# Performance work log

Measured on AMD Instinct MI355X. Metric: run time of the kernel, lower is better.

Reference implementation:

```python
import jax, jax.numpy as jnp
import numpy as np

KERNELSIZE = 9


def generate_pe(pos_num, d_num):
    pos = jnp.arange(pos_num, dtype=jnp.float32)[:, None]
    d_i = jnp.arange(0, d_num + 1, 2, dtype=jnp.float32)[None, :]
    ang = pos / jnp.power(jnp.float32(10000.0), d_i / d_num)  # [pos, ceil((d+1)/2)]
    pe = jnp.zeros((pos_num, d_num), dtype=jnp.float32)
    n_even = pe[:, 0::2].shape[1]
    n_odd = pe[:, 1::2].shape[1]
    pe = pe.at[:, 0::2].set(jnp.sin(ang)[:, :n_even])
    pe = pe.at[:, 1::2].set(jnp.cos(ang)[:, :n_odd])
    return pe


def nearest_idx(in_size, out_size):
    # torch F.interpolate(mode='nearest'): src = floor(dst * in/out)
    return jnp.floor(jnp.arange(out_size) * (in_size / out_size)).astype(jnp.int32)


def setup_inputs() -> dict:
    N, K, C_in, C_out, ks = 30000, 16, 256, 128, KERNELSIZE
    key = jax.random.key(0)
    k0, k1, k2, k3, k4, k5, k6, k7 = jax.random.split(key, 8)
    return {
        "ndata": jax.random.normal(k0, (N, C_in), jnp.float32),
        "neighbors": jax.random.randint(k1, (N, K), 0, N),
        "W_lin": jax.random.normal(k2, (C_out, C_in), jnp.float32) * 0.05,
        "b_lin": jax.random.normal(k3, (C_out,), jnp.float32) * 0.05,
        "weight": jax.random.normal(k4, (C_out, ks), jnp.float32),
        "bias": jax.random.normal(k5, (C_out,), jnp.float32),
        "W_res": jax.random.normal(k6, (C_out, C_in), jnp.float32) * 0.05,
        "b_res": jax.random.normal(k7, (C_out,), jnp.float32) * 0.05,
    }


def reference(ndata, neighbors, W_lin, b_lin, weight, bias, W_res, b_res):
    N = ndata.shape[0]
    C_out, ks = weight.shape
    feat = ndata @ W_lin.T + b_lin                              # [N, D]
    # mailbox = in-neighbor features + self-loop (dgl.add_self_loop)
    mailbox = jnp.concatenate([feat[neighbors], feat[:, None, :]], axis=1)  # [N, S, D]
    S = mailbox.shape[1]
    x = jnp.sort(mailbox, axis=1)                                # sort along neighbor dim
    idx = nearest_idx(ks, S)
    pe = generate_pe(ks, C_out)                                  # [ks, D]
    x = x + pe[idx][None, :, :]                                  # interpolated PE
    w_local = weight[:, idx].T                                   # [S, D] interpolated weight
    Xf = jnp.fft.fft(x, axis=1)
    Wf = jnp.fft.fft(w_local, axis=0)
    y = jnp.fft.ifft(Xf * jnp.conj(Wf)[None, :, :], axis=1).real  # circular correlation
    h = y.sum(axis=1) + bias                                     # [N, D]
    return h + ndata @ W_res.T + b_res
```

## Files before the change

kernel.cpp:

```cpp
#include <hip/hip_runtime.h>
#include <math.h>

#define N_NODES 30000
#define K_NBR   16
#define C_IN    256
#define C_OUT   128
#define KS      9
#define S_MB    17

typedef __attribute__((ext_vector_type(4))) float f32x4;
typedef __attribute__((ext_vector_type(8))) short bf16x8;

static __device__ __forceinline__ ushort f2bf(float f) {
    uint u = __builtin_bit_cast(uint, f);
    u += 0x7fffu + ((u >> 16) & 1u);
    return (ushort)(u >> 16);
}

__global__ __launch_bounds__(256)
void pcg_prep(const float* __restrict__ W_lin,
              const float* __restrict__ W_res,
              const float* __restrict__ weight,
              const float* __restrict__ b_lin,
              const float* __restrict__ bias,
              const float* __restrict__ b_res,
              ushort* __restrict__ Bf,
              float* __restrict__ Ws,
              float* __restrict__ Cd) {
    if (blockIdx.x == 32) {
        int d = threadIdx.x;
        if (d >= C_OUT) return;
        float freq = powf(10000.0f, -(float)(d & ~1) / (float)C_OUT);
        float ws = 0.f, p = 0.f;
        for (int s = 0; s < S_MB; ++s) {
            int idx = (int)floorf((float)s * (9.0f / 17.0f));
            ws += weight[d * KS + idx];
            float ang = (float)idx * freq;
            p += (d & 1) ? cosf(ang) : sinf(ang);
        }
        Ws[d] = ws;
        Cd[d] = ws * ((float)(K_NBR + 1) * b_lin[d] + p) + bias[d] + b_res[d];
        return;
    }
    const int tt     = blockIdx.x * 256 + threadIdx.x;
    const int col_lo = tt & 15;
    const int ksub   = (tt >> 4) & 3;
    const int colhi  = (tt >> 6) & 15;
    const int kc     = tt >> 10;
    const int col    = colhi * 16 + col_lo;
    const int k0     = kc * 32 + ksub * 8;
    const float* Wr = (col < C_OUT)
        ? &W_lin[(size_t)col * C_IN + k0]
        : &W_res[(size_t)(col - C_OUT) * C_IN + k0];
    const float4 w0 = *reinterpret_cast<const float4*>(Wr);
    const float4 w1 = *reinterpret_cast<const float4*>(Wr + 4);
    ushort b[8] = { f2bf(w0.x), f2bf(w0.y), f2bf(w0.z), f2bf(w0.w),
                    f2bf(w1.x), f2bf(w1.y), f2bf(w1.z), f2bf(w1.w) };
    *reinterpret_cast<uint4*>(&Bf[(size_t)tt * 8]) =
        *reinterpret_cast<const uint4*>(b);
}

__global__ __launch_bounds__(256)
void pcg_mfma(const float* __restrict__ ndata,
              const ushort* __restrict__ Bf,
              ushort* __restrict__ F) {
    __shared__ short sA[16384];

    const int t  = threadIdx.x;
    const int n0 = blockIdx.x * 64;

#pragma unroll
    for (int i = 0; i < 16; ++i) {
        const int v    = i * 256 + t;
        const int row  = v >> 6;
        const int k0   = (v & 63) * 4;
        float4 a = make_float4(0.f, 0.f, 0.f, 0.f);
        if (n0 + row < N_NODES)
            a = *reinterpret_cast<const float4*>(
                    &ndata[(size_t)(n0 + row) * C_IN + k0]);
        const int kc   = k0 >> 5;
        const int rg   = row >> 4;
        const int l    = (row & 15) | (((k0 >> 3) & 3) << 4);
        const int half = (k0 >> 2) & 1;
        uint2 w;
        w.x = (uint)f2bf(a.x) | ((uint)f2bf(a.y) << 16);
        w.y = (uint)f2bf(a.z) | ((uint)f2bf(a.w) << 16);
        *reinterpret_cast<uint2*>(&sA[(kc * 4 + rg) * 512 + l * 8 + half * 4]) = w;
    }
    __syncthreads();

    const int wave = t >> 6;
    const int l    = t & 63;

    f32x4 acc[4][4] = {};

#pragma unroll
    for (int kc = 0; kc < 8; ++kc) {
        bf16x8 a[4];
#pragma unroll
        for (int rg = 0; rg < 4; ++rg)
            a[rg] = *reinterpret_cast<const bf16x8*>(
                        &sA[(kc * 4 + rg) * 512 + l * 8]);
        bf16x8 b[4];
#pragma unroll
        for (int cg = 0; cg < 4; ++cg)
            b[cg] = *reinterpret_cast<const bf16x8*>(
                        &Bf[((size_t)(kc * 16 + wave * 4 + cg) * 64 + l) * 8]);
#pragma unroll
        for (int rg = 0; rg < 4; ++rg)
#pragma unroll
            for (int cg = 0; cg < 4; ++cg)
                acc[rg][cg] = __builtin_amdgcn_mfma_f32_16x16x32_bf16(
                                  a[rg], b[cg], acc[rg][cg], 0, 0, 0);
    }

    const int colw = wave * 64 + (l & 15);
    const int rl   = (l >> 4) * 4;
#pragma unroll
    for (int rg = 0; rg < 4; ++rg) {
#pragma unroll
        for (int cg = 0; cg < 4; ++cg) {
            const int col = colw + cg * 16;
#pragma unroll
            for (int j = 0; j < 4; ++j) {
                const int row = n0 + rg * 16 + rl + j;
                if (row < N_NODES)
                    F[(size_t)row * 256 + col] = f2bf(acc[rg][cg][j]);
            }
        }
    }
}

__global__ __launch_bounds__(256)
void pcg_gather(const int* __restrict__ neighbors,
                const ushort* __restrict__ F,
                const float* __restrict__ Ws,
                const float* __restrict__ Cd,
                float* __restrict__ out) {
    __shared__ int snb[64];
    const int t = threadIdx.x;
    if (t < 64) snb[t] = neighbors[(size_t)blockIdx.x * 64 + t];
    __syncthreads();

    const int g = t >> 6;
    const int l = t & 63;
    const int n = blockIdx.x * 4 + g;

    const ushort* Frow = F + (size_t)n * 256;
    uint u = *reinterpret_cast<const uint*>(&Frow[2 * l]);
    float a0 = __builtin_bit_cast(float, u << 16);
    float a1 = __builtin_bit_cast(float, u & 0xffff0000u);

#pragma unroll
    for (int k = 0; k < K_NBR; ++k) {
        const int m = snb[g * 16 + k];
        uint v = *reinterpret_cast<const uint*>(&F[(size_t)m * 256 + 2 * l]);
        a0 += __builtin_bit_cast(float, v << 16);
        a1 += __builtin_bit_cast(float, v & 0xffff0000u);
    }

    uint r = *reinterpret_cast<const uint*>(&Frow[128 + 2 * l]);
    float r0 = __builtin_bit_cast(float, r << 16);
    float r1 = __builtin_bit_cast(float, r & 0xffff0000u);

    float2 ws = *reinterpret_cast<const float2*>(&Ws[2 * l]);
    float2 cd = *reinterpret_cast<const float2*>(&Cd[2 * l]);

    float2 o;
    o.x = ws.x * a0 + r0 + cd.x;
    o.y = ws.y * a1 + r1 + cd.y;
    *reinterpret_cast<float2*>(&out[(size_t)n * C_OUT + 2 * l]) = o;
}

extern "C" void kernel_launch(void* const* d_in, const int* in_sizes, int n_in,
                              void* d_out, int out_size, void* d_ws, size_t ws_size,
                              hipStream_t stream) {
    const float* ndata     = (const float*)d_in[0];
    const int*   neighbors = (const int*)  d_in[1];
    const float* W_lin     = (const float*)d_in[2];
    const float* b_lin     = (const float*)d_in[3];
    const float* weight    = (const float*)d_in[4];
    const float* bias      = (const float*)d_in[5];
    const float* W_res     = (const float*)d_in[6];
    const float* b_res     = (const float*)d_in[7];
    float* out = (float*)d_out;

    ushort* F  = (ushort*)d_ws;
    ushort* Bf = F + (size_t)N_NODES * 256;
    float*  Ws = (float*)(Bf + 65536);
    float*  Cd = Ws + C_OUT;

    pcg_prep<<<33, 256, 0, stream>>>(W_lin, W_res, weight, b_lin, bias, b_res,
                                     Bf, Ws, Cd);
    pcg_mfma<<<(N_NODES + 63) / 64, 256, 0, stream>>>(ndata, Bf, F);
    pcg_gather<<<N_NODES / 4, 256, 0, stream>>>(neighbors, F, Ws, Cd, out);
}
```

Before: 43.84 us.

## Fold Ws scale, residual and constant into GEMM epilogue; gather pre-scaled rows

The GEMM epilogue now multiplies the linear output by the per-channel weight sum and writes two bf16 arrays: the scaled neighbour features and a per-node term that already includes the self contribution, the residual and the constants. Column groups are remapped so each wave holds matching linear and residual columns. The gather kernel then only sums pre-scaled rows and stores with nontemporal writes, dropping the residual and Ws/Cd loads. Nontemporal loads are also used for ndata. Output bytes stay the same, but the extra bf16 rounding after scaling changes numerical error slightly.

```diff
diff --git a/kernel.cpp b/kernel.cpp
--- a/kernel.cpp
+++ b/kernel.cpp
@@ -9,6 +9,7 @@
 #define S_MB    17
 
 typedef __attribute__((ext_vector_type(4))) float f32x4;
+typedef __attribute__((ext_vector_type(2))) float f32x2;
 typedef __attribute__((ext_vector_type(8))) short bf16x8;
 
 static __device__ __forceinline__ ushort f2bf(float f) {
@@ -52,8 +53,8 @@
     const float* Wr = (col < C_OUT)
         ? &W_lin[(size_t)col * C_IN + k0]
         : &W_res[(size_t)(col - C_OUT) * C_IN + k0];
-    const float4 w0 = *reinterpret_cast<const float4*>(Wr);
-    const float4 w1 = *reinterpret_cast<const float4*>(Wr + 4);
+    const f32x4 w0 = *reinterpret_cast<const f32x4*>(Wr);
+    const f32x4 w1 = *reinterpret_cast<const f32x4*>(Wr + 4);
     ushort b[8] = { f2bf(w0.x), f2bf(w0.y), f2bf(w0.z), f2bf(w0.w),
                     f2bf(w1.x), f2bf(w1.y), f2bf(w1.z), f2bf(w1.w) };
     *reinterpret_cast<uint4*>(&Bf[(size_t)tt * 8]) =
@@ -63,7 +64,10 @@
 __global__ __launch_bounds__(256)
 void pcg_mfma(const float* __restrict__ ndata,
               const ushort* __restrict__ Bf,
-              ushort* __restrict__ F) {
+              const float* __restrict__ Ws,
+              const float* __restrict__ Cd,
+              ushort* __restrict__ Gs,
+              ushort* __restrict__ Pc) {
     __shared__ short sA[16384];
 
     const int t  = threadIdx.x;
@@ -74,10 +78,10 @@
         const int v    = i * 256 + t;
         const int row  = v >> 6;
         const int k0   = (v & 63) * 4;
-        float4 a = make_float4(0.f, 0.f, 0.f, 0.f);
+        f32x4 a = {0.f, 0.f, 0.f, 0.f};
         if (n0 + row < N_NODES)
-            a = *reinterpret_cast<const float4*>(
-                    &ndata[(size_t)(n0 + row) * C_IN + k0]);
+            a = __builtin_nontemporal_load(reinterpret_cast<const f32x4*>(
+                    &ndata[(size_t)(n0 + row) * C_IN + k0]));
         const int kc   = k0 >> 5;
         const int rg   = row >> 4;
         const int l    = (row & 15) | (((k0 >> 3) & 3) << 4);
@@ -92,6 +96,11 @@
     const int wave = t >> 6;
     const int l    = t & 63;
 
+    const int ch0 = 2 * wave;
+    const int ch1 = 2 * wave + 1;
+    const int ch2 = 8 + 2 * wave;
+    const int ch3 = 9 + 2 * wave;
+
     f32x4 acc[4][4] = {};
 
 #pragma unroll
@@ -102,10 +111,10 @@
             a[rg] = *reinterpret_cast<const bf16x8*>(
                         &sA[(kc * 4 + rg) * 512 + l * 8]);
         bf16x8 b[4];
-#pragma unroll
-        for (int cg = 0; cg < 4; ++cg)
-            b[cg] = *reinterpret_cast<const bf16x8*>(
-                        &Bf[((size_t)(kc * 16 + wave * 4 + cg) * 64 + l) * 8]);
+        b[0] = *reinterpret_cast<const bf16x8*>(&Bf[((size_t)(kc * 16 + ch0) * 64 + l) * 8]);
+        b[1] = *reinterpret_cast<const bf16x8*>(&Bf[((size_t)(kc * 16 + ch1) * 64 + l) * 8]);
+        b[2] = *reinterpret_cast<const bf16x8*>(&Bf[((size_t)(kc * 16 + ch2) * 64 + l) * 8]);
+        b[3] = *reinterpret_cast<const bf16x8*>(&Bf[((size_t)(kc * 16 + ch3) * 64 + l) * 8]);
 #pragma unroll
         for (int rg = 0; rg < 4; ++rg)
 #pragma unroll
@@ -114,18 +123,24 @@
                                   a[rg], b[cg], acc[rg][cg], 0, 0, 0);
     }
 
-    const int colw = wave * 64 + (l & 15);
-    const int rl   = (l >> 4) * 4;
+    const int cl  = l & 15;
+    const int c0  = wave * 32 + cl;
+    const int c1  = wave * 32 + 16 + cl;
+    const float ws0 = Ws[c0], ws1 = Ws[c1];
+    const float cd0 = Cd[c0], cd1 = Cd[c1];
+    const int rl  = (l >> 4) * 4;
 #pragma unroll
     for (int rg = 0; rg < 4; ++rg) {
 #pragma unroll
-        for (int cg = 0; cg < 4; ++cg) {
-            const int col = colw + cg * 16;
-#pragma unroll
-            for (int j = 0; j < 4; ++j) {
-                const int row = n0 + rg * 16 + rl + j;
-                if (row < N_NODES)
-                    F[(size_t)row * 256 + col] = f2bf(acc[rg][cg][j]);
+        for (int j = 0; j < 4; ++j) {
+            const int row = n0 + rg * 16 + rl + j;
+            if (row < N_NODES) {
+                const float gs0 = ws0 * acc[rg][0][j];
+                const float gs1 = ws1 * acc[rg][1][j];
+                Gs[(size_t)row * C_OUT + c0] = f2bf(gs0);
+                Gs[(size_t)row * C_OUT + c1] = f2bf(gs1);
+                Pc[(size_t)row * C_OUT + c0] = f2bf(gs0 + acc[rg][2][j] + cd0);
+                Pc[(size_t)row * C_OUT + c1] = f2bf(gs1 + acc[rg][3][j] + cd1);
             }
         }
     }
@@ -133,9 +148,8 @@
 
 __global__ __launch_bounds__(256)
 void pcg_gather(const int* __restrict__ neighbors,
-                const ushort* __restrict__ F,
-                const float* __restrict__ Ws,
-                const float* __restrict__ Cd,
+                const ushort* __restrict__ Gs,
+                const ushort* __restrict__ Pc,
                 float* __restrict__ out) {
     __shared__ int snb[64];
     const int t = threadIdx.x;
@@ -146,30 +160,21 @@
     const int l = t & 63;
     const int n = blockIdx.x * 4 + g;
 
-    const ushort* Frow = F + (size_t)n * 256;
-    uint u = *reinterpret_cast<const uint*>(&Frow[2 * l]);
-    float a0 = __builtin_bit_cast(float, u << 16);
-    float a1 = __builtin_bit_cast(float, u & 0xffff0000u);
+    uint p = *reinterpret_cast<const uint*>(&Pc[(size_t)n * C_OUT + 2 * l]);
+    float a0 = __builtin_bit_cast(float, p << 16);
+    float a1 = __builtin_bit_cast(float, p & 0xffff0000u);
 
 #pragma unroll
     for (int k = 0; k < K_NBR; ++k) {
         const int m = snb[g * 16 + k];
-        uint v = *reinterpret_cast<const uint*>(&F[(size_t)m * 256 + 2 * l]);
+        uint v = *reinterpret_cast<const uint*>(&Gs[(size_t)m * C_OUT + 2 * l]);
         a0 += __builtin_bit_cast(float, v << 16);
         a1 += __builtin_bit_cast(float, v & 0xffff0000u);
     }
 
-    uint r = *reinterpret_cast<const uint*>(&Frow[128 + 2 * l]);
-    float r0 = __builtin_bit_cast(float, r << 16);
-    float r1 = __builtin_bit_cast(float, r & 0xffff0000u);
-
-    float2 ws = *reinterpret_cast<const float2*>(&Ws[2 * l]);
-    float2 cd = *reinterpret_cast<const float2*>(&Cd[2 * l]);
-
-    float2 o;
-    o.x = ws.x * a0 + r0 + cd.x;
-    o.y = ws.y * a1 + r1 + cd.y;
-    *reinterpret_cast<float2*>(&out[(size_t)n * C_OUT + 2 * l]) = o;
+    f32x2 o = {a0, a1};
+    __builtin_nontemporal_store(o, reinterpret_cast<f32x2*>(
+        &out[(size_t)n * C_OUT + 2 * l]));
 }
 
 extern "C" void kernel_launch(void* const* d_in, const int* in_sizes, int n_in,
@@ -185,13 +190,14 @@
     const float* b_res     = (const float*)d_in[7];
     float* out = (float*)d_out;
 
-    ushort* F  = (ushort*)d_ws;
-    ushort* Bf = F + (size_t)N_NODES * 256;
-    float*  Ws = (float*)(Bf + 65536);
+    ushort* Bf = (ushort*)d_ws;
+    ushort* Gq = Bf + 65536;
+    ushort* Pq = Gq + (size_t)N_NODES * C_OUT;
+    float*  Ws = (float*)(Pq + (size_t)N_NODES * C_OUT);
     float*  Cd = Ws + C_OUT;
 
     pcg_prep<<<33, 256, 0, stream>>>(W_lin, W_res, weight, b_lin, bias, b_res,
                                      Bf, Ws, Cd);
-    pcg_mfma<<<(N_NODES + 63) / 64, 256, 0, stream>>>(ndata, Bf, F);
-    pcg_gather<<<N_NODES / 4, 256, 0, stream>>>(neighbors, F, Ws, Cd, out);
-}
+    pcg_mfma<<<(N_NODES + 63) / 64, 256, 0, stream>>>(ndata, Bf, Ws, Cd, Gq, Pq);
+    pcg_gather<<<N_NODES / 4, 256, 0, stream>>>(neighbors, Gq, Pq, out);
+}
```

Measured after the change: 48.10 us. 1.1x slower.
